# Optimization experiments

Hardware: AMD Instinct MI355X
Metric: run time of the kernel (lower is better)

The kernel has to match this reference:

```python
import jax, jax.numpy as jnp
import numpy as np

EMB = 1024
HEADS = 16
HEAD_DIM = EMB // HEADS  # 64


def setup_inputs() -> dict:
    key = jax.random.key(0)
    ks = jax.random.split(key, 11)
    B, S = 2, 2048
    scale = 1.0 / np.sqrt(EMB)
    inp = {
        "xv": jax.random.normal(ks[0], (B, S, EMB), jnp.float32),
        "xk": jax.random.normal(ks[1], (B, S, EMB), jnp.float32),
        "xq": jax.random.normal(ks[2], (B, S, EMB), jnp.float32),
        "Wq": jax.random.normal(ks[3], (EMB, EMB), jnp.float32) * scale,
        "bq": jax.random.normal(ks[4], (EMB,), jnp.float32) * 0.01,
        "Wk": jax.random.normal(ks[5], (EMB, EMB), jnp.float32) * scale,
        "bk": jax.random.normal(ks[6], (EMB,), jnp.float32) * 0.01,
        "Wv": jax.random.normal(ks[7], (EMB, EMB), jnp.float32) * scale,
        "bv": jax.random.normal(ks[8], (EMB,), jnp.float32) * 0.01,
        "Wo": jax.random.normal(ks[9], (EMB, EMB), jnp.float32) * scale,
        "bo": jax.random.normal(ks[10], (EMB,), jnp.float32) * 0.01,
    }
    return inp


def reference(xv, xk, xq, Wq, bq, Wk, bk, Wv, bv, Wo, bo):
    B, S, E = xq.shape
    H, D = HEADS, HEAD_DIM
    # projections (x @ W + b), split into heads: [B,S,H,D]
    Q = (xq @ Wq + bq).reshape(B, S, H, D)
    K = (xk @ Wk + bk).reshape(B, S, H, D)
    V = (xv @ Wv + bv).reshape(B, S, H, D)
    # scaled dot-product attention per head (vectorized over heads)
    scores = jnp.einsum("bqhd,bkhd->bhqk", Q, K) / jnp.sqrt(jnp.float32(D))
    attn = jax.nn.softmax(scores, axis=-1)
    ctx = jnp.einsum("bhqk,bkhd->bqhd", attn, V).reshape(B, S, E)
    return ctx @ Wo + bo
```

## Files before the change

### kernel.cpp

```cpp
#include <hip/hip_runtime.h>
#include <hip/hip_bf16.h>

typedef __hip_bfloat16 bf16;
typedef __attribute__((ext_vector_type(8))) short short8;
typedef __attribute__((ext_vector_type(4))) short short4v;
typedef __attribute__((ext_vector_type(4))) float floatx4;

#define MFMA16 __builtin_amdgcn_mfma_f32_16x16x32_bf16
#define BARRIER __builtin_amdgcn_s_barrier
#define SCHEDB0() __builtin_amdgcn_sched_barrier(0)
#define SETPRIO __builtin_amdgcn_s_setprio


__device__ __forceinline__ void gl16(const void* g, void* l) {
    __builtin_amdgcn_global_load_lds(
        (const __attribute__((address_space(1))) void*)g,
        (__attribute__((address_space(3))) void*)l, 16, 0, 0);
}

__global__ __launch_bounds__(256) void prep_k(const float* __restrict__ w0,
                                              const float* __restrict__ w1,
                                              const float* __restrict__ w2,
                                              const float* __restrict__ w3,
                                              bf16* __restrict__ wdst,
                                              const float* __restrict__ x0,
                                              const float* __restrict__ x1,
                                              const float* __restrict__ x2,
                                              bf16* __restrict__ xdst) {
    int bid = blockIdx.x, tid = threadIdx.x;
    if (bid < 4096) {
        const float* srcs[4] = {w0, w1, w2, w3};
        int z = bid >> 10, by = (bid >> 5) & 31, bx = bid & 31;
        const float* src = srcs[z];
        bf16* d = wdst + (size_t)z * 1024 * 1024;
        __shared__ float t[32][33];
        int tx = tid & 31, ty = tid >> 5;
        int x0c = bx * 32, y0 = by * 32;
#pragma unroll
        for (int i = 0; i < 4; i++)
            t[ty + i * 8][tx] = src[(size_t)(y0 + ty + i * 8) * 1024 + x0c + tx];
        __syncthreads();
#pragma unroll
        for (int i = 0; i < 4; i++)
            d[(size_t)(x0c + ty + i * 8) * 1024 + y0 + tx] =
                __float2bfloat16(t[tx][ty + i * 8]);
    } else {
        int ib = bid - 4096;
        int zc = ib >> 11, blk = ib & 2047;
        const float* srcs[3] = {x0, x1, x2};
        const float* src = srcs[zc];
        bf16* d = xdst + (size_t)zc * (4096 * 1024);
        size_t i = (size_t)blk * 256 + tid;
        const float4* s4 = (const float4*)src + i * 2;
        float4 a = s4[0], b = s4[1];
        union { __hip_bfloat162 h2[4]; short8 s; } pk;
        pk.h2[0] = __float22bfloat162_rn(make_float2(a.x, a.y));
        pk.h2[1] = __float22bfloat162_rn(make_float2(a.z, a.w));
        pk.h2[2] = __float22bfloat162_rn(make_float2(b.x, b.y));
        pk.h2[3] = __float22bfloat162_rn(make_float2(b.z, b.w));
        *(short8*)&d[i * 8] = pk.s;
    }
}

__global__ __launch_bounds__(256) void qkv_k(const bf16* __restrict__ xb,
                                             const bf16* __restrict__ wt,
                                             const float* __restrict__ bq,
                                             const float* __restrict__ bk,
                                             const float* __restrict__ bv,
                                             bf16* __restrict__ Qw,
                                             bf16* __restrict__ Kw,
                                             bf16* __restrict__ Vt) {
    __shared__ __align__(16) bf16 lA[3][128 * 32];
    __shared__ __align__(16) bf16 lB[3][128 * 32];
    int z = blockIdx.z;
    const bf16* A = xb + (size_t)z * (4096 * 1024);
    const bf16* Bt = wt + (size_t)z * (1024 * 1024);
    const float* bias = (z == 0) ? bq : (z == 1) ? bk : bv;
    int m0 = blockIdx.x * 128, n0 = blockIdx.y * 128;
    int tid = threadIdx.x, wave = tid >> 6, lane = tid & 63;
    int lm = lane & 15, quad = lane >> 4;
    int wm = wave >> 1, wn = wave & 1;
    int swb = quad ^ ((lm >> 1) & 3);

    floatx4 acc[4][4];
#pragma unroll
    for (int i = 0; i < 4; i++)
#pragma unroll
        for (int j = 0; j < 4; j++) acc[i][j] = (floatx4){0.f, 0.f, 0.f, 0.f};

    auto stage = [&](int bufi, int kt) {
#pragma unroll
        for (int q2 = 0; q2 < 2; q2++) {
            int slot0 = wave * 128 + q2 * 64;
            int r = (slot0 + lane) >> 2;
            int c = (lane & 3) ^ ((r >> 1) & 3);
            gl16(&A[(size_t)(m0 + r) * 1024 + kt * 32 + c * 8],
                 &lA[bufi][slot0 * 8]);
            gl16(&Bt[(size_t)(n0 + r) * 1024 + kt * 32 + c * 8],
                 &lB[bufi][slot0 * 8]);
        }
    };

    auto compute = [&](int cur) {
        short8 af[4], bfr[4];
#pragma unroll
        for (int ms = 0; ms < 4; ms++) {
            int r = wm * 64 + ms * 16 + lm;
            af[ms] = *(const short8*)&lA[cur][(r * 4 + swb) * 8];
        }
#pragma unroll
        for (int ns = 0; ns < 4; ns++) {
            int r = wn * 64 + ns * 16 + lm;
            bfr[ns] = *(const short8*)&lB[cur][(r * 4 + swb) * 8];
        }
        SETPRIO(1);
#pragma unroll
        for (int ms = 0; ms < 4; ms++)
#pragma unroll
            for (int ns = 0; ns < 4; ns++)
                acc[ms][ns] = MFMA16(af[ms], bfr[ns], acc[ms][ns], 0, 0, 0);
        SETPRIO(0);
    };

    stage(0, 0);
    stage(1, 1);
    for (int kt = 0; kt < 32; kt++) {
        int cur = kt % 3;
        BARRIER();
        if (kt < 30) {
            stage((kt + 2) % 3, kt + 2);
            asm volatile("s_waitcnt vmcnt(8)" ::: "memory");
        } else if (kt == 30) {
            asm volatile("s_waitcnt vmcnt(4)" ::: "memory");
        } else {
            asm volatile("s_waitcnt vmcnt(0)" ::: "memory");
        }
        BARRIER();
        SCHEDB0();
        compute(cur);
    }

    bf16* dstQK = (z == 0) ? Qw : Kw;
    float scale = (z == 0) ? 0.125f * 1.44269504f : 1.0f;
#pragma unroll
    for (int ms = 0; ms < 4; ms++) {
        int rowb = m0 + wm * 64 + ms * 16 + quad * 4;
        int bb = rowb >> 11, s0 = rowb & 2047;
#pragma unroll
        for (int ns = 0; ns < 4; ns++) {
            int col = n0 + wn * 64 + ns * 16 + lm;
            float bvv = bias[col];
            int hh = col >> 6, d = col & 63;
            if (z < 2) {
#pragma unroll
                for (int rr = 0; rr < 4; rr++) {
                    float v = (acc[ms][ns][rr] + bvv) * scale;
                    dstQK[((((size_t)bb * 16 + hh) * 2048 + s0 + rr) << 6) + d] =
                        __float2bfloat16(v);
                }
            } else {
                short4v pk;
#pragma unroll
                for (int rr = 0; rr < 4; rr++) {
                    bf16 h = __float2bfloat16(acc[ms][ns][rr] + bvv);
                    pk[rr] = *(short*)&h;
                }
                *(short4v*)&Vt[((((size_t)bb * 16 + hh) * 64 + d) << 11) + s0] = pk;
            }
        }
    }
}

__global__ __launch_bounds__(256) void outproj_k(const bf16* __restrict__ ctx,
                                                 const bf16* __restrict__ wot,
                                                 const float* __restrict__ bo,
                                                 float* __restrict__ out) {
    __shared__ __align__(16) bf16 lA[2][64 * 32];
    __shared__ __align__(16) bf16 lB[2][64 * 32];
    int m0 = blockIdx.x * 64, n0 = blockIdx.y * 64;
    int tid = threadIdx.x, wave = tid >> 6, lane = tid & 63;
    int lm = lane & 15, quad = lane >> 4;
    int wm = wave >> 1, wn = wave & 1;
    int swb = quad ^ ((lm >> 1) & 3);

    floatx4 acc[2][2];
#pragma unroll
    for (int i = 0; i < 2; i++)
#pragma unroll
        for (int j = 0; j < 2; j++) acc[i][j] = (floatx4){0.f, 0.f, 0.f, 0.f};

    auto stage = [&](int bufi, int kt) {
        int slot0 = wave * 64;
        int r = (slot0 + lane) >> 2;
        int c = (lane & 3) ^ ((r >> 1) & 3);
        gl16(&ctx[(size_t)(m0 + r) * 1024 + kt * 32 + c * 8],
             &lA[bufi][slot0 * 8]);
        gl16(&wot[(size_t)(n0 + r) * 1024 + kt * 32 + c * 8],
             &lB[bufi][slot0 * 8]);
    };

    auto compute = [&](int cur) {
        short8 af[2], bfr[2];
#pragma unroll
        for (int ms = 0; ms < 2; ms++) {
            int r = wm * 32 + ms * 16 + lm;
            af[ms] = *(const short8*)&lA[cur][(r * 4 + swb) * 8];
        }
#pragma unroll
        for (int ns = 0; ns < 2; ns++) {
            int r = wn * 32 + ns * 16 + lm;
            bfr[ns] = *(const short8*)&lB[cur][(r * 4 + swb) * 8];
        }
        SETPRIO(1);
#pragma unroll
        for (int ms = 0; ms < 2; ms++)
#pragma unroll
            for (int ns = 0; ns < 2; ns++)
                acc[ms][ns] = MFMA16(af[ms], bfr[ns], acc[ms][ns], 0, 0, 0);
        SETPRIO(0);
    };

    stage(0, 0);
    for (int kt = 0; kt < 31; kt++) {
        int cur = kt & 1;
        BARRIER();
        stage(cur ^ 1, kt + 1);
        asm volatile("s_waitcnt vmcnt(2)" ::: "memory");
        BARRIER();
        SCHEDB0();
        compute(cur);
    }
    BARRIER();
    asm volatile("s_waitcnt vmcnt(0)" ::: "memory");
    BARRIER();
    SCHEDB0();
    compute(1);

#pragma unroll
    for (int ms = 0; ms < 2; ms++) {
        int rowb = m0 + wm * 32 + ms * 16 + quad * 4;
#pragma unroll
        for (int ns = 0; ns < 2; ns++) {
            int col = n0 + wn * 32 + ns * 16 + lm;
            float bvv = bo[col];
#pragma unroll
            for (int rr = 0; rr < 4; rr++)
                out[(size_t)(rowb + rr) * 1024 + col] = acc[ms][ns][rr] + bvv;
        }
    }
}

__global__ __launch_bounds__(512, 4) void attn_k(const bf16* __restrict__ Q,
                                                 const bf16* __restrict__ K,
                                                 const bf16* __restrict__ Vt,
                                                 bf16* __restrict__ ctx) {
    __shared__ __align__(16) bf16 lK[2][128 * 64];
    __shared__ __align__(16) bf16 lV[2][64 * 128];
    __shared__ float scrL[4][32];
    int bh = blockIdx.x, qt = blockIdx.y;
    int b = bh >> 4, h = bh & 15;
    const bf16* Qh = Q + (size_t)bh * (2048 * 64);
    const bf16* Kh = K + (size_t)bh * (2048 * 64);
    const bf16* Vh = Vt + (size_t)bh * (64 * 2048);
    int tid = threadIdx.x, wave = tid >> 6, lane = tid & 63;
    int lm = lane & 15, quad = lane >> 4;
    int s7 = lm & 7;
    int wq = wave >> 1, wk = wave & 1;

    short8 qf[2][2];
#pragma unroll
    for (int qblk = 0; qblk < 2; qblk++) {
        int qrow = qt * 128 + wq * 32 + qblk * 16 + lm;
        qf[qblk][0] = *(const short8*)&Qh[(size_t)qrow * 64 + quad * 8];
        qf[qblk][1] = *(const short8*)&Qh[(size_t)qrow * 64 + 32 + quad * 8];
    }

    short8 onesf;
#pragma unroll
    for (int i = 0; i < 8; i++) onesf[i] = (short)0x3F80;

    floatx4 o[2][4];
#pragma unroll
    for (int i = 0; i < 2; i++)
#pragma unroll
        for (int j = 0; j < 4; j++) o[i][j] = (floatx4){0.f, 0.f, 0.f, 0.f};
    floatx4 accL[2];
#pragma unroll
    for (int i = 0; i < 2; i++) accL[i] = (floatx4){0.f, 0.f, 0.f, 0.f};

    auto stage = [&](int bufi, int kt) {
#pragma unroll
        for (int q2 = 0; q2 < 2; q2++) {
            int slot0 = wave * 128 + q2 * 64;
            int r = (slot0 + lane) >> 3;
            int c = (lane & 7) ^ (r & 7);
            gl16(&Kh[(size_t)(kt * 128 + r) * 64 + c * 8], &lK[bufi][slot0 * 8]);
        }
#pragma unroll
        for (int q2 = 0; q2 < 2; q2++) {
            int slot0 = wave * 128 + q2 * 64;
            int s = slot0 + lane;
            int r = s >> 4, cl = s & 15;
            int c = cl ^ (r & 7);
            gl16(&Vh[(size_t)r * 2048 + kt * 128 + c * 8], &lV[bufi][slot0 * 8]);
        }
    };

    auto read_kf = [&](int cur, int half, short8 kf[2][2]) {
#pragma unroll
        for (int ksub = 0; ksub < 2; ksub++) {
            int r = wk * 64 + half * 32 + ksub * 16 + lm;
#pragma unroll
            for (int ds = 0; ds < 2; ds++)
                kf[ksub][ds] = *(const short8*)
                    &lK[cur][(r * 8 + ((ds * 4 + quad) ^ s7)) * 8];
        }
    };
    auto qk = [&](short8 kf[2][2], floatx4 s[2][2]) {
#pragma unroll
        for (int i = 0; i < 2; i++)
#pragma unroll
            for (int j = 0; j < 2; j++) s[i][j] = (floatx4){0.f, 0.f, 0.f, 0.f};
        SETPRIO(1);
#pragma unroll
        for (int qblk = 0; qblk < 2; qblk++)
#pragma unroll
            for (int ksub = 0; ksub < 2; ksub++) {
                s[qblk][ksub] = MFMA16(kf[ksub][0], qf[qblk][0], s[qblk][ksub], 0, 0, 0);
                s[qblk][ksub] = MFMA16(kf[ksub][1], qf[qblk][1], s[qblk][ksub], 0, 0, 0);
            }
        SETPRIO(0);
    };
    auto mkpz = [&](floatx4 s[2][2], short8 pz[2]) {
#pragma unroll
        for (int qblk = 0; qblk < 2; qblk++) {
            union { short4v h[2]; short8 s8; } up;
#pragma unroll
            for (int ksub = 0; ksub < 2; ksub++) {
                float p0 = __builtin_amdgcn_exp2f(s[qblk][ksub][0]);
                float p1 = __builtin_amdgcn_exp2f(s[qblk][ksub][1]);
                float p2 = __builtin_amdgcn_exp2f(s[qblk][ksub][2]);
                float p3 = __builtin_amdgcn_exp2f(s[qblk][ksub][3]);
                union { __hip_bfloat162 b2[2]; short4v s4; } c;
                c.b2[0] = __float22bfloat162_rn(make_float2(p0, p1));
                c.b2[1] = __float22bfloat162_rn(make_float2(p2, p3));
                up.h[ksub] = c.s4;
            }
            pz[qblk] = up.s8;
        }
    };
    auto read_vfz = [&](int cur, int half, short8 vfz[4]) {
#pragma unroll
        for (int dblk = 0; dblk < 4; dblk++) {
            int d = dblk * 16 + lm;
            union { short4v h[2]; short8 s8; } uv;
#pragma unroll
            for (int ksub = 0; ksub < 2; ksub++) {
                int c = wk * 8 + half * 4 + ksub * 2 + (quad >> 1);
                uv.h[ksub] = *(const short4v*)
                    &lV[cur][(d * 16 + (c ^ s7)) * 8 + (quad & 1) * 4];
            }
            vfz[dblk] = uv.s8;
        }
    };
    auto pv = [&](short8 pz[2], short8 vfz[4]) {
        SETPRIO(1);
#pragma unroll
        for (int qblk = 0; qblk < 2; qblk++) {
            accL[qblk] = MFMA16(pz[qblk], onesf, accL[qblk], 0, 0, 0);
#pragma unroll
            for (int dblk = 0; dblk < 4; dblk++)
                o[qblk][dblk] = MFMA16(pz[qblk], vfz[dblk], o[qblk][dblk], 0, 0, 0);
        }
        SETPRIO(0);
    };

    auto compute = [&](int cur) {
        short8 kf0[2][2], kf1[2][2];
        floatx4 s0[2][2], s1[2][2];
        short8 pz0[2], pz1[2];
        short8 vfz0[4], vfz1[4];

        read_kf(cur, 0, kf0);
        qk(kf0, s0);
        read_kf(cur, 1, kf1);
        mkpz(s0, pz0);
        qk(kf1, s1);
        read_vfz(cur, 0, vfz0);
        pv(pz0, vfz0);
        mkpz(s1, pz1);
        read_vfz(cur, 1, vfz1);
        pv(pz1, vfz1);
    };

    stage(0, 0);
    for (int kt = 0; kt < 15; kt++) {
        int cur = kt & 1;
        BARRIER();
        stage(cur ^ 1, kt + 1);
        asm volatile("s_waitcnt vmcnt(4)" ::: "memory");
        BARRIER();
        SCHEDB0();
        compute(cur);
    }
    BARRIER();
    asm volatile("s_waitcnt vmcnt(0)" ::: "memory");
    BARRIER();
    SCHEDB0();
    compute(1);

    __syncthreads();
    float* scrO = (float*)&lK[0][0];
    if (wk == 1) {
#pragma unroll
        for (int qblk = 0; qblk < 2; qblk++) {
#pragma unroll
            for (int dblk = 0; dblk < 4; dblk++)
#pragma unroll
                for (int rr = 0; rr < 4; rr++)
                    scrO[wq * 2048 + (qblk * 16 + quad * 4 + rr) * 64 +
                         dblk * 16 + lm] = o[qblk][dblk][rr];
#pragma unroll
            for (int rr = 0; rr < 4; rr++)
                scrL[wq][qblk * 16 + quad * 4 + rr] = accL[qblk][rr];
        }
    }
    __syncthreads();
    if (wk == 0) {
#pragma unroll
        for (int qblk = 0; qblk < 2; qblk++) {
            float inv[4];
#pragma unroll
            for (int rr = 0; rr < 4; rr++)
                inv[rr] = 1.f / (accL[qblk][rr] +
                                 scrL[wq][qblk * 16 + quad * 4 + rr]);
#pragma unroll
            for (int dblk = 0; dblk < 4; dblk++) {
                int e = h * 64 + dblk * 16 + lm;
#pragma unroll
                for (int rr = 0; rr < 4; rr++) {
                    int srow = qt * 128 + wq * 32 + qblk * 16 + quad * 4 + rr;
                    float of = o[qblk][dblk][rr] +
                               scrO[wq * 2048 + (qblk * 16 + quad * 4 + rr) * 64 +
                                    dblk * 16 + lm];
                    ctx[(size_t)(b * 2048 + srow) * 1024 + e] =
                        __float2bfloat16(of * inv[rr]);
                }
            }
        }
    }
}

extern "C" void kernel_launch(void* const* d_in, const int* in_sizes, int n_in,
                              void* d_out, int out_size, void* d_ws, size_t ws_size,
                              hipStream_t stream) {
    const float* xv = (const float*)d_in[0];
    const float* xk = (const float*)d_in[1];
    const float* xq = (const float*)d_in[2];
    const float* Wq = (const float*)d_in[3];
    const float* bq = (const float*)d_in[4];
    const float* Wk = (const float*)d_in[5];
    const float* bk = (const float*)d_in[6];
    const float* Wv = (const float*)d_in[7];
    const float* bv = (const float*)d_in[8];
    const float* Wo = (const float*)d_in[9];
    const float* bo = (const float*)d_in[10];
    float* out = (float*)d_out;
    bf16* ws = (bf16*)d_ws;

    const size_t MB1 = 1024 * 1024;
    bf16* wt  = ws;
    bf16* Qw  = ws + 4 * MB1;
    bf16* Kw  = ws + 8 * MB1;
    bf16* Vt  = ws + 12 * MB1;
    bf16* ctx = ws + 16 * MB1;
    bf16* xb  = ws + 20 * MB1;

    hipLaunchKernelGGL(prep_k, dim3(10240), dim3(256), 0, stream,
                       Wq, Wk, Wv, Wo, wt, xq, xk, xv, xb);

    hipLaunchKernelGGL(qkv_k, dim3(32, 8, 3), dim3(256), 0, stream,
                       xb, wt, bq, bk, bv, Qw, Kw, Vt);

    hipLaunchKernelGGL(attn_k, dim3(32, 16), dim3(512), 0, stream, Qw, Kw, Vt, ctx);

    hipLaunchKernelGGL(outproj_k, dim3(64, 16), dim3(256), 0, stream,
                       ctx, wt + 3 * MB1, bo, out);
}
```

Measured before the change: 216.2 us.

## Load V fragments directly from global memory instead of staging through LDS

```diff
diff --git a/kernel.cpp b/kernel.cpp
--- a/kernel.cpp
+++ b/kernel.cpp
@@ -255,7 +255,6 @@
                                                  const bf16* __restrict__ Vt,
                                                  bf16* __restrict__ ctx) {
     __shared__ __align__(16) bf16 lK[2][128 * 64];
-    __shared__ __align__(16) bf16 lV[2][64 * 128];
     __shared__ float scrL[4][32];
     int bh = blockIdx.x, qt = blockIdx.y;
     int b = bh >> 4, h = bh & 15;
@@ -288,7 +287,7 @@
 #pragma unroll
     for (int i = 0; i < 2; i++) accL[i] = (floatx4){0.f, 0.f, 0.f, 0.f};
 
-    auto stage = [&](int bufi, int kt) {
+    auto stageK = [&](int bufi, int kt) {
 #pragma unroll
         for (int q2 = 0; q2 < 2; q2++) {
             int slot0 = wave * 128 + q2 * 64;
@@ -296,17 +295,25 @@
             int c = (lane & 7) ^ (r & 7);
             gl16(&Kh[(size_t)(kt * 128 + r) * 64 + c * 8], &lK[bufi][slot0 * 8]);
         }
-#pragma unroll
-        for (int q2 = 0; q2 < 2; q2++) {
-            int slot0 = wave * 128 + q2 * 64;
-            int s = slot0 + lane;
-            int r = s >> 4, cl = s & 15;
-            int c = cl ^ (r & 7);
-            gl16(&Vh[(size_t)r * 2048 + kt * 128 + c * 8], &lV[bufi][slot0 * 8]);
-        }
-    };
-
-    auto read_kf = [&](int cur, int half, short8 kf[2][2]) {
+    };
+
+    auto loadV = [&](int kt, int half, short8 vfz[4]) {
+#pragma unroll
+        for (int dblk = 0; dblk < 4; dblk++) {
+            int d = dblk * 16 + lm;
+            union { short4v hh[2]; short8 s8; } uv;
+#pragma unroll
+            for (int ksub = 0; ksub < 2; ksub++) {
+                uv.hh[ksub] = *(const short4v*)
+                    &Vh[(size_t)d * 2048 + kt * 128 + wk * 64 + half * 32 +
+                        ksub * 16 + quad * 4];
+            }
+            vfz[dblk] = uv.s8;
+        }
+    };
+
+    auto do_half = [&](int cur, int half, short8 vfz[4]) {
+        short8 kf[2][2];
 #pragma unroll
         for (int ksub = 0; ksub < 2; ksub++) {
             int r = wk * 64 + half * 32 + ksub * 16 + lm;
@@ -315,8 +322,7 @@
                 kf[ksub][ds] = *(const short8*)
                     &lK[cur][(r * 8 + ((ds * 4 + quad) ^ s7)) * 8];
         }
-    };
-    auto qk = [&](short8 kf[2][2], floatx4 s[2][2]) {
+        floatx4 s[2][2];
 #pragma unroll
         for (int i = 0; i < 2; i++)
 #pragma unroll
@@ -330,11 +336,11 @@
                 s[qblk][ksub] = MFMA16(kf[ksub][1], qf[qblk][1], s[qblk][ksub], 0, 0, 0);
             }
         SETPRIO(0);
-    };
-    auto mkpz = [&](floatx4 s[2][2], short8 pz[2]) {
+
+        short8 pz[2];
 #pragma unroll
         for (int qblk = 0; qblk < 2; qblk++) {
-            union { short4v h[2]; short8 s8; } up;
+            union { short4v hh[2]; short8 s8; } up;
 #pragma unroll
             for (int ksub = 0; ksub < 2; ksub++) {
                 float p0 = __builtin_amdgcn_exp2f(s[qblk][ksub][0]);
@@ -344,26 +350,11 @@
                 union { __hip_bfloat162 b2[2]; short4v s4; } c;
                 c.b2[0] = __float22bfloat162_rn(make_float2(p0, p1));
                 c.b2[1] = __float22bfloat162_rn(make_float2(p2, p3));
-                up.h[ksub] = c.s4;
+                up.hh[ksub] = c.s4;
             }
             pz[qblk] = up.s8;
         }
-    };
-    auto read_vfz = [&](int cur, int half, short8 vfz[4]) {
-#pragma unroll
-        for (int dblk = 0; dblk < 4; dblk++) {
-            int d = dblk * 16 + lm;
-            union { short4v h[2]; short8 s8; } uv;
-#pragma unroll
-            for (int ksub = 0; ksub < 2; ksub++) {
-                int c = wk * 8 + half * 4 + ksub * 2 + (quad >> 1);
-                uv.h[ksub] = *(const short4v*)
-                    &lV[cur][(d * 16 + (c ^ s7)) * 8 + (quad & 1) * 4];
-            }
-            vfz[dblk] = uv.s8;
-        }
-    };
-    auto pv = [&](short8 pz[2], short8 vfz[4]) {
+
         SETPRIO(1);
 #pragma unroll
         for (int qblk = 0; qblk < 2; qblk++) {
@@ -375,41 +366,21 @@
         SETPRIO(0);
     };
 
-    auto compute = [&](int cur) {
-        short8 kf0[2][2], kf1[2][2];
-        floatx4 s0[2][2], s1[2][2];
-        short8 pz0[2], pz1[2];
-        short8 vfz0[4], vfz1[4];
-
-        read_kf(cur, 0, kf0);
-        qk(kf0, s0);
-        read_kf(cur, 1, kf1);
-        mkpz(s0, pz0);
-        qk(kf1, s1);
-        read_vfz(cur, 0, vfz0);
-        pv(pz0, vfz0);
-        mkpz(s1, pz1);
-        read_vfz(cur, 1, vfz1);
-        pv(pz1, vfz1);
-    };
-
-    stage(0, 0);
-    for (int kt = 0; kt < 15; kt++) {
-        int cur = kt & 1;
-        BARRIER();
-        stage(cur ^ 1, kt + 1);
-        asm volatile("s_waitcnt vmcnt(4)" ::: "memory");
-        BARRIER();
-        SCHEDB0();
-        compute(cur);
-    }
-    BARRIER();
+    stageK(0, 0);
     asm volatile("s_waitcnt vmcnt(0)" ::: "memory");
     BARRIER();
-    SCHEDB0();
-    compute(1);
-
-    __syncthreads();
+    for (int kt = 0; kt < 16; kt++) {
+        int cur = kt & 1;
+        short8 vfz[4];
+        loadV(kt, 0, vfz);
+        if (kt < 15) stageK(cur ^ 1, kt + 1);
+        do_half(cur, 0, vfz);
+        loadV(kt, 1, vfz);
+        do_half(cur, 1, vfz);
+        asm volatile("s_waitcnt vmcnt(0)" ::: "memory");
+        BARRIER();
+    }
+
     float* scrO = (float*)&lK[0][0];
     if (wk == 1) {
 #pragma unroll
```

After: 291.9 us. 1.35x slower.
